# Kernel optimization log

Hardware: AMD Instinct MI355X
Metric: run time of the kernel (lower is better)

The kernel has to match this reference:

```python
import jax, jax.numpy as jnp
import numpy as np
import math

# Module constants (from __init__ defaults / chosen init_kwargs)
B = 4            # hand_batch_size
C = 8            # num_cameras
BC = B * C       # camera batch
R = 256          # resolution
NB = 64          # num_bins
BIN = 0.0136     # bin_size
FOV = 33.0       # degrees
DCS = 0.001      # camera_sensor_distance
SIGMA_BIN = 3.0  # self.sigma for soft binning


def _masks():
    fov_rad = FOV * math.pi / 180.0
    scale = math.tan(fov_rad / 2.0)
    center_scale = scale * (1.0 - 1.0 / R)
    lin = jnp.linspace(-center_scale, center_scale, R, dtype=jnp.float32)
    xg, yg = jnp.meshgrid(lin, lin, indexing='xy')
    fm = jnp.stack([xg, -yg, -jnp.ones((R, R), jnp.float32)], axis=2)
    film_mask = -fm / jnp.linalg.norm(fm, axis=2, keepdims=True)  # [R,R,3]
    cos_mask = 1.0 / jnp.sqrt(xg * xg + yg * yg + 1.0)            # [R,R]
    return film_mask, cos_mask


def setup_inputs() -> dict:
    key = jax.random.key(0)
    k1, k2 = jax.random.split(key)
    film_mask, cos_mask = _masks()
    # per-pixel interpolated vertex normals (pre-normalization, as dr.interpolate output)
    normals = jax.random.normal(k1, (BC, R, R, 3), dtype=jnp.float32)
    # per-pixel camera-space intersection points; z ~ 0.5 m so depths fall mid-histogram
    intersections = jax.random.normal(k2, (BC, R, R, 3), dtype=jnp.float32) * 0.1 \
        + jnp.array([0.0, 0.0, 0.5], dtype=jnp.float32)
    return {"normals": normals, "intersections": intersections,
            "film_mask": film_mask, "cos_mask": cos_mask}


def reference(normals, intersections, film_mask, cos_mask):
    width = 2.0 * math.tan(FOV * math.pi / 360.0)
    # cosine foreshortening w.r.t. film ray directions
    dots = jnp.clip(jnp.einsum('ijk,bijk->bij', film_mask, normals), 0.0, 1.0)
    # laser origin offset by 2 * camera_sensor_distance along +x
    laser_points = intersections - jnp.array([2.0 * DCS, 0.0, 0.0], dtype=intersections.dtype)
    laser_distances = jnp.linalg.norm(laser_points, axis=3)  # [BC,R,R]
    laser_tan = jnp.sqrt(laser_points[..., 0] ** 2 + laser_points[..., 1] ** 2) / laser_points[..., 2]
    sig = math.tan(math.radians(21.5)) / 1.4
    laser_mask = jnp.exp(-laser_tan ** 2 / (2.0 * sig * sig))
    dots = dots * laser_mask
    radiance = dots / laser_distances / laser_distances / math.pi \
        * (width * width) * (cos_mask ** 3) / float(R * R)      # [BC,R,R]
    depths = (jnp.linalg.norm(intersections, axis=3) + laser_distances) / 2.0
    d_bin = depths / BIN                                         # [BC,R,R]
    b = jnp.arange(NB, dtype=jnp.float32)                        # [NB]
    # soft bin kernel: sigmoid(s*(d-b)) - sigmoid(s*(d-b-1)), [BC,R,R,NB]
    x = d_bin[..., None] - b
    kernels = jax.nn.sigmoid(SIGMA_BIN * x) - jax.nn.sigmoid(SIGMA_BIN * (x - 1.0))
    # histogram accumulation over all pixels -> per-camera transient [BC,NB]
    transients = jnp.einsum('bijk,bij->bk', kernels, radiance)
    return transients
```

## Files before the change

kernel.cpp:

```cpp
#include <hip/hip_runtime.h>
#include <math.h>

#define NPIX    65536
#define NBINS   64
#define NBATCH  32
#define SPLIT   32
#define BLOCKT  128
#define PXPT    4
#define ITERS   (NPIX / SPLIT / (BLOCKT * PXPT))
#define HSTRIDE 65
#define LDSN    (BLOCKT * HSTRIDE)
#define WIN     8

#define E3          20.085536923187668f
#define THREE_LOG2E 4.328085122666891f

__global__ __launch_bounds__(BLOCKT) void spad_hist_kernel(
    const float* __restrict__ normals,
    const float* __restrict__ inters,
    const float* __restrict__ film,
    const float* __restrict__ cosm,
    float* __restrict__ ws,
    float kconst, float lmask_c, float half_inv_bin)
{
    __shared__ float hist[LDSN];
    const int tid = threadIdx.x;
    for (int i = tid; i < LDSN; i += BLOCKT) hist[i] = 0.0f;
    __syncthreads();

    const int b = blockIdx.x & (NBATCH - 1);
    const int chunk = blockIdx.x / NBATCH;
    const int pix0 = chunk * (NPIX / SPLIT);
    const int base = tid * HSTRIDE;

    auto accum = [&](float nx, float ny, float nz,
                     float ix, float iy, float iz,
                     float fx, float fy, float fz, float cm) {
        float dt = fx * nx + fy * ny + fz * nz;
        dt = fminf(fmaxf(dt, 0.0f), 1.0f);
        float lx = ix - 0.002f;
        float lxy2 = lx * lx + iy * iy;
        float l2 = lxy2 + iz * iz;
        float ld = __builtin_amdgcn_sqrtf(l2);
        float lm = __builtin_amdgcn_exp2f(lmask_c * lxy2 * __builtin_amdgcn_rcpf(iz * iz));
        float cm3 = cm * cm * cm;
        float r = dt * lm * kconst * cm3 * __builtin_amdgcn_rcpf(l2);
        float di = __builtin_amdgcn_sqrtf(ix * ix + iy * iy + iz * iz);
        float d = (di + ld) * half_inv_bin;

        int j0 = (int)floorf(d);
        j0 = j0 < 3 ? 3 : (j0 > 59 ? 59 : j0);
        const int k0 = j0 - 3;
        float e = __builtin_amdgcn_exp2f(((float)k0 - d) * THREE_LOG2E);
        float sPrev = __builtin_amdgcn_rcpf(1.0f + e);
        const int p = base + k0;
        #pragma unroll
        for (int m = 0; m < WIN; ++m) {
            e *= E3;
            float sCur = __builtin_amdgcn_rcpf(1.0f + e);
            hist[p + m] += r * (sPrev - sCur);
            sPrev = sCur;
        }
    };

    #pragma unroll
    for (int it = 0; it < ITERS; ++it) {
        const int pp = pix0 + (it * BLOCKT + tid) * PXPT;
        const float4* n4 = (const float4*)(normals + ((size_t)b * NPIX + pp) * 3);
        const float4* i4 = (const float4*)(inters  + ((size_t)b * NPIX + pp) * 3);
        const float4* f4 = (const float4*)(film + (size_t)pp * 3);
        const float4  c4 = *(const float4*)(cosm + pp);
        float4 n0 = n4[0], n1 = n4[1], n2 = n4[2];
        float4 i0 = i4[0], i1 = i4[1], i2 = i4[2];
        float4 f0 = f4[0], f1 = f4[1], f2 = f4[2];

        accum(n0.x, n0.y, n0.z, i0.x, i0.y, i0.z, f0.x, f0.y, f0.z, c4.x);
        accum(n0.w, n1.x, n1.y, i0.w, i1.x, i1.y, f0.w, f1.x, f1.y, c4.y);
        accum(n1.z, n1.w, n2.x, i1.z, i1.w, i2.x, f1.z, f1.w, f2.x, c4.z);
        accum(n2.y, n2.z, n2.w, i2.y, i2.z, i2.w, f2.y, f2.z, f2.w, c4.w);
    }
    __syncthreads();

    if (tid < NBINS) {
        float s = 0.0f;
        for (int t = 0; t < BLOCKT; ++t) s += hist[t * HSTRIDE + tid];
        ws[(size_t)blockIdx.x * NBINS + tid] = s;
    }
}

__global__ __launch_bounds__(256) void spad_reduce_kernel(
    const float* __restrict__ ws, float* __restrict__ out)
{
    const int o = blockIdx.x * 256 + threadIdx.x;
    const int b = o >> 6;
    const int k = o & 63;
    float s = 0.0f;
    #pragma unroll
    for (int c = 0; c < SPLIT; ++c)
        s += ws[((size_t)(c * NBATCH + b)) * NBINS + k];
    out[o] = s;
}

extern "C" void kernel_launch(void* const* d_in, const int* in_sizes, int n_in,
                              void* d_out, int out_size, void* d_ws, size_t ws_size,
                              hipStream_t stream) {
    const float* normals = (const float*)d_in[0];
    const float* inters  = (const float*)d_in[1];
    const float* film    = (const float*)d_in[2];
    const float* cosm    = (const float*)d_in[3];
    float* out = (float*)d_out;
    float* ws  = (float*)d_ws;

    const double fov_rad = 33.0 * M_PI / 180.0;
    const double width = 2.0 * tan(fov_rad / 2.0);
    const double kconst_d = width * width / M_PI / 65536.0;
    const double sig = tan(21.5 * M_PI / 180.0) / 1.4;
    const double log2e = 1.4426950408889634;
    const double lmask_c_d = -log2e / (2.0 * sig * sig);
    const double half_inv_bin_d = 0.5 / 0.0136;

    spad_hist_kernel<<<NBATCH * SPLIT, BLOCKT, 0, stream>>>(
        normals, inters, film, cosm, ws,
        (float)kconst_d, (float)lmask_c_d, (float)half_inv_bin_d);

    spad_reduce_kernel<<<(NBATCH * NBINS) / 256, 256, 0, stream>>>(ws, out);
}
```

Before: 94.82 us.

## Vectorize per-thread histogram updates with aligned float4 windows and parallel final reduction

```diff
diff --git a/kernel.cpp b/kernel.cpp
--- a/kernel.cpp
+++ b/kernel.cpp
@@ -8,14 +8,13 @@
 #define BLOCKT  128
 #define PXPT    4
 #define ITERS   (NPIX / SPLIT / (BLOCKT * PXPT))
-#define HSTRIDE 65
+#define HSTRIDE 68
 #define LDSN    (BLOCKT * HSTRIDE)
-#define WIN     8
+#define WIN     12
 
-#define E3          20.085536923187668f
 #define THREE_LOG2E 4.328085122666891f
 
-__global__ __launch_bounds__(BLOCKT) void spad_hist_kernel(
+__global__ __launch_bounds__(BLOCKT, 2) void spad_hist_kernel(
     const float* __restrict__ normals,
     const float* __restrict__ inters,
     const float* __restrict__ film,
@@ -25,7 +24,11 @@
 {
     __shared__ float hist[LDSN];
     const int tid = threadIdx.x;
-    for (int i = tid; i < LDSN; i += BLOCKT) hist[i] = 0.0f;
+    {
+        float4* h4 = (float4*)&hist[tid * HSTRIDE];
+        #pragma unroll
+        for (int i = 0; i < HSTRIDE / 4; ++i) h4[i] = make_float4(0.f, 0.f, 0.f, 0.f);
+    }
     __syncthreads();
 
     const int b = blockIdx.x & (NBATCH - 1);
@@ -33,35 +36,11 @@
     const int pix0 = chunk * (NPIX / SPLIT);
     const int base = tid * HSTRIDE;
 
-    auto accum = [&](float nx, float ny, float nz,
-                     float ix, float iy, float iz,
-                     float fx, float fy, float fz, float cm) {
-        float dt = fx * nx + fy * ny + fz * nz;
-        dt = fminf(fmaxf(dt, 0.0f), 1.0f);
-        float lx = ix - 0.002f;
-        float lxy2 = lx * lx + iy * iy;
-        float l2 = lxy2 + iz * iz;
-        float ld = __builtin_amdgcn_sqrtf(l2);
-        float lm = __builtin_amdgcn_exp2f(lmask_c * lxy2 * __builtin_amdgcn_rcpf(iz * iz));
-        float cm3 = cm * cm * cm;
-        float r = dt * lm * kconst * cm3 * __builtin_amdgcn_rcpf(l2);
-        float di = __builtin_amdgcn_sqrtf(ix * ix + iy * iy + iz * iz);
-        float d = (di + ld) * half_inv_bin;
-
-        int j0 = (int)floorf(d);
-        j0 = j0 < 3 ? 3 : (j0 > 59 ? 59 : j0);
-        const int k0 = j0 - 3;
-        float e = __builtin_amdgcn_exp2f(((float)k0 - d) * THREE_LOG2E);
-        float sPrev = __builtin_amdgcn_rcpf(1.0f + e);
-        const int p = base + k0;
-        #pragma unroll
-        for (int m = 0; m < WIN; ++m) {
-            e *= E3;
-            float sCur = __builtin_amdgcn_rcpf(1.0f + e);
-            hist[p + m] += r * (sPrev - sCur);
-            sPrev = sCur;
-        }
-    };
+    const float E3P[13] = {
+        1.0f, 20.085536923187668f, 403.4287934927351f, 8103.083927575384f,
+        162754.79141900392f, 3269017.372472111f, 65659969.13733051f,
+        1318815734.4832146f, 26489122129.843472f, 532048240601.79865f,
+        10686474581524.462f, 214643579785916.06f, 4311231547115195.0f };
 
     #pragma unroll
     for (int it = 0; it < ITERS; ++it) {
@@ -74,17 +53,85 @@
         float4 i0 = i4[0], i1 = i4[1], i2 = i4[2];
         float4 f0 = f4[0], f1 = f4[1], f2 = f4[2];
 
-        accum(n0.x, n0.y, n0.z, i0.x, i0.y, i0.z, f0.x, f0.y, f0.z, c4.x);
-        accum(n0.w, n1.x, n1.y, i0.w, i1.x, i1.y, f0.w, f1.x, f1.y, c4.y);
-        accum(n1.z, n1.w, n2.x, i1.z, i1.w, i2.x, f1.z, f1.w, f2.x, c4.z);
-        accum(n2.y, n2.z, n2.w, i2.y, i2.z, i2.w, f2.y, f2.z, f2.w, c4.w);
+        float NX[4] = {n0.x, n0.w, n1.z, n2.y}, NY[4] = {n0.y, n1.x, n1.w, n2.z},
+              NZ[4] = {n0.z, n1.y, n2.x, n2.w};
+        float IX[4] = {i0.x, i0.w, i1.z, i2.y}, IY[4] = {i0.y, i1.x, i1.w, i2.z},
+              IZ[4] = {i0.z, i1.y, i2.x, i2.w};
+        float FX[4] = {f0.x, f0.w, f1.z, f2.y}, FY[4] = {f0.y, f1.x, f1.w, f2.z},
+              FZ[4] = {f0.z, f1.y, f2.x, f2.w};
+        float CM[4] = {c4.x, c4.y, c4.z, c4.w};
+
+        float R[4];
+        int   K0[4];
+        float S[4][13];
+
+        #pragma unroll
+        for (int p = 0; p < 4; ++p) {
+            float dt = FX[p] * NX[p] + FY[p] * NY[p] + FZ[p] * NZ[p];
+            dt = fminf(fmaxf(dt, 0.0f), 1.0f);
+            float lx = IX[p] - 0.002f;
+            float lxy2 = lx * lx + IY[p] * IY[p];
+            float l2 = lxy2 + IZ[p] * IZ[p];
+            float ld = __builtin_amdgcn_sqrtf(l2);
+            float lm = __builtin_amdgcn_exp2f(
+                lmask_c * lxy2 * __builtin_amdgcn_rcpf(IZ[p] * IZ[p]));
+            float cm3 = CM[p] * CM[p] * CM[p];
+            R[p] = dt * lm * kconst * cm3 * __builtin_amdgcn_rcpf(l2);
+            float di = __builtin_amdgcn_sqrtf(
+                IX[p] * IX[p] + IY[p] * IY[p] + IZ[p] * IZ[p]);
+            float d = (di + ld) * half_inv_bin;
+
+            int j0 = (int)floorf(d);
+            j0 = j0 < 4 ? 4 : (j0 > 56 ? 56 : j0);
+            int k0 = (j0 - 4) & ~3;
+            K0[p] = k0;
+            float e0 = __builtin_amdgcn_exp2f(((float)k0 - d) * THREE_LOG2E);
+            #pragma unroll
+            for (int m = 0; m < 13; ++m)
+                S[p][m] = __builtin_amdgcn_rcpf(1.0f + e0 * E3P[m]);
+        }
+
+        #pragma unroll
+        for (int p = 0; p < 4; ++p) {
+            float4* hp = (float4*)&hist[base + K0[p]];
+            float4 a = hp[0], bb = hp[1], c = hp[2];
+            float r = R[p];
+            a.x  += r * (S[p][0]  - S[p][1]);
+            a.y  += r * (S[p][1]  - S[p][2]);
+            a.z  += r * (S[p][2]  - S[p][3]);
+            a.w  += r * (S[p][3]  - S[p][4]);
+            bb.x += r * (S[p][4]  - S[p][5]);
+            bb.y += r * (S[p][5]  - S[p][6]);
+            bb.z += r * (S[p][6]  - S[p][7]);
+            bb.w += r * (S[p][7]  - S[p][8]);
+            c.x  += r * (S[p][8]  - S[p][9]);
+            c.y  += r * (S[p][9]  - S[p][10]);
+            c.z  += r * (S[p][10] - S[p][11]);
+            c.w  += r * (S[p][11] - S[p][12]);
+            hp[0] = a; hp[1] = bb; hp[2] = c;
+        }
     }
     __syncthreads();
 
-    if (tid < NBINS) {
-        float s = 0.0f;
-        for (int t = 0; t < BLOCKT; ++t) s += hist[t * HSTRIDE + tid];
-        ws[(size_t)blockIdx.x * NBINS + tid] = s;
+    const int g = tid & 15;
+    const int h = tid >> 4;
+    float4 acc = make_float4(0.f, 0.f, 0.f, 0.f);
+    #pragma unroll
+    for (int j = 0; j < 16; ++j) {
+        float4 v = *(const float4*)&hist[(h + 8 * j) * HSTRIDE + 4 * g];
+        acc.x += v.x; acc.y += v.y; acc.z += v.z; acc.w += v.w;
+    }
+    __syncthreads();
+    *(float4*)&hist[tid * 4] = acc;
+    __syncthreads();
+    if (tid < 16) {
+        float4 s4 = make_float4(0.f, 0.f, 0.f, 0.f);
+        #pragma unroll
+        for (int hh = 0; hh < 8; ++hh) {
+            float4 v = *(const float4*)&hist[hh * 64 + tid * 4];
+            s4.x += v.x; s4.y += v.y; s4.z += v.z; s4.w += v.w;
+        }
+        *(float4*)&ws[(size_t)blockIdx.x * NBINS + tid * 4] = s4;
     }
 }
 
```

Measured after the change: 92.99 us. Within noise of the previous version (-1.9%).
